# Kernel optimization log

Hardware: AMD Instinct MI355X
Metric: run time of the kernel (lower is better)

## Reference

```python
import jax, jax.numpy as jnp
import numpy as np

SIZE = 161          # odd box size (init arg 160 -> 161)
INPUT_SIZE = 8
BATCH = 256
MARGIN = 3          # VOXEL_SPREAD_MARGIN


def _radial_expansion(grid):
    # verbatim numpy port of SparseVolumeReconstructionLinear.radial_expansion
    bz = grid.shape[0]
    bz2 = bz // 2
    mask1 = grid == -1
    ls = np.linspace(-bz2, bz2, bz)
    lsx = np.linspace(0, bz2, bz // 2 + 1)
    z, y, x = np.meshgrid(ls, ls, lsx)
    c = np.zeros((int(np.sum(mask1)), 3))
    c[:, 0] = x[mask1]
    c[:, 1] = y[mask1]
    c[:, 2] = z[mask1]
    norm = np.sqrt(np.sum(np.square(c), axis=1))
    c_ = np.round(c / norm[:, None]).astype(int)
    c = c.astype(int)
    c[:, 1:] += bz2
    c_ = c - c_
    g = grid[c_[:, 2], c_[:, 1], c_[:, 0]]
    mask2 = g >= 0
    grid[c[mask2, 2], c[mask2, 1], c[mask2, 0]] = g[mask2]


def _build_grid3d_index(size):
    bz = size
    bz_2 = bz // 2
    zz = (np.arange(bz) - bz_2) ** 2
    yy = (np.arange(bz) - bz_2) ** 2
    xx = np.arange(bz_2 + 1) ** 2
    mask = (zz[:, None, None] + yy[None, :, None] + xx[None, None, :]) <= bz_2 ** 2
    # C-order enumeration matches grid_iterator(z, y, x) ordering
    idx = np.cumsum(mask.ravel()).reshape(mask.shape) - 1
    grid = np.where(mask, idx, -1).astype(np.int64)
    m = MARGIN
    bzm = bz + 2 * m
    gm = np.full((bzm, bzm, bzm // 2 + 1), -1, dtype=np.int64)
    gm[m:-m, m:-m, :-m] = grid
    for _ in range(5):
        _radial_expansion(gm)
    return gm, int(mask.sum())


def _rand_rotations(key, n):
    q = jax.random.normal(key, (n, 4))
    q = q / jnp.linalg.norm(q, axis=1, keepdims=True)
    w, x, y, z = q[:, 0], q[:, 1], q[:, 2], q[:, 3]
    R = jnp.stack([
        1 - 2 * (y * y + z * z), 2 * (x * y - z * w), 2 * (x * z + y * w),
        2 * (x * y + z * w), 1 - 2 * (x * x + z * z), 2 * (y * z - x * w),
        2 * (x * z - y * w), 2 * (y * z + x * w), 1 - 2 * (x * x + y * y),
    ], axis=-1).reshape(n, 3, 3)
    return R.astype(jnp.float32)


def setup_inputs() -> dict:
    key = jax.random.key(0)
    k1, k2, k3, k4 = jax.random.split(key, 4)
    grid3d_index, weight_count = _build_grid3d_index(SIZE)
    weight = jax.random.normal(k1, (weight_count, INPUT_SIZE, 2), dtype=jnp.float32) * 1e-3
    bias = jax.random.normal(k2, (weight_count, 2), dtype=jnp.float32) * 1e-3
    inp = jax.random.normal(k3, (BATCH, INPUT_SIZE), dtype=jnp.float32)
    rot = _rand_rotations(k4, BATCH)
    # half-plane 2D Fourier coords (x >= 0), P = SIZE * (SIZE//2 + 1)
    ys, xs = np.meshgrid(np.arange(SIZE) - SIZE // 2, np.arange(SIZE // 2 + 1), indexing='ij')
    coord = np.stack([xs.ravel(), ys.ravel()], axis=-1).astype(np.float32)
    return {
        'input': inp,
        'weight': weight,
        'bias': bias,
        'grid3d_index': jnp.asarray(grid3d_index),
        'rot_matrices': rot,
        'grid2d_coord': jnp.asarray(coord),
        'max_r': SIZE // 2,
    }


def reference(input, weight, bias, grid3d_index, rot_matrices, grid2d_coord, max_r):
    # input: (B, D); weight: (W, D, 2); bias: (W, 2)
    # grid2d_coord: (P, 2) as (x, y); rot_matrices: (B, 3, 3)
    bz = grid3d_index.shape[0]
    bz2 = bz // 2
    mr = min(int(max_r), (bz - 2 * MARGIN) // 2)
    P = grid2d_coord.shape[0]
    # rotate the z=0 plane into 3D Fourier space: (B, P, 3) as (x, y, z)
    c2 = jnp.pad(grid2d_coord, ((0, 0), (0, 1)))
    c = jnp.einsum('bij,pj->bpi', rot_matrices, c2)
    # Hermitian symmetry: flip to x >= 0 half-grid, conjugate
    flip = c[..., 0] < 0
    c = jnp.where(flip[..., None], -c, c)
    valid = jnp.sum(grid2d_coord ** 2, axis=-1) <= float(mr * mr)  # (P,)
    c = jnp.where(valid[None, :, None], c, 0.0)
    f = jnp.floor(c)
    t = c - f                      # trilinear fractions (B, P, 3)
    fi = f.astype(jnp.int32)
    out = jnp.zeros((c.shape[0], P, 2), dtype=input.dtype)
    for dx in (0, 1):
        wx = t[..., 0] if dx else 1.0 - t[..., 0]
        for dy in (0, 1):
            wy = t[..., 1] if dy else 1.0 - t[..., 1]
            for dz in (0, 1):
                wz = t[..., 2] if dz else 1.0 - t[..., 2]
                xi = fi[..., 0] + dx
                yi = fi[..., 1] + dy + bz2
                zi = fi[..., 2] + dz + bz2
                j = grid3d_index[zi, yi, xi]        # (B, P) voxel ids, -1 = empty
                jm = jnp.maximum(j, 0)
                v = jnp.einsum('bd,bpdc->bpc', input, weight[jm]) + bias[jm]
                v = jnp.where((j >= 0)[..., None], v, 0.0)
                out = out + (wx * wy * wz)[..., None] * v
    imag_sign = jnp.where(flip, -1.0, 1.0)
    out = out * jnp.stack([jnp.ones_like(imag_sign), imag_sign], axis=-1)
    return jnp.where(valid[None, :, None], out, 0.0)
```

## Files before the change

### kernel.cpp

```cpp
#include <hip/hip_runtime.h>

#define BZ    167
#define BZ2   83
#define NX    84
#define NCELL (BZ * BZ * NX)
#define SYC   NX
#define SZC   (NX * BZ)
#define NXC   81
#define NYC   161
#define NTX   21
#define NTZ   11
#define NBX   51

static __device__ __forceinline__ unsigned f2bf(float f) {
    unsigned u = __float_as_uint(f);
    return (u + 0x7FFFu + ((u >> 16) & 1u)) >> 16;
}
static __device__ __forceinline__ float bf_lo(unsigned u) {
    return __uint_as_float(u << 16);
}
static __device__ __forceinline__ float bf_hi(unsigned u) {
    return __uint_as_float(u & 0xFFFF0000u);
}

typedef _Float16 h2 __attribute__((ext_vector_type(2)));
static __device__ __forceinline__ h2 u2h(unsigned u) {
    union { unsigned u; h2 h; } x; x.u = u; return x.h;
}
static __device__ __forceinline__ unsigned f2h2(float a, float b) {
    union { h2 h; unsigned u; } x;
    x.h.x = (_Float16)a; x.h.y = (_Float16)b;
    return x.u;
}

__global__ __launch_bounds__(256) void pack_allh(
    const float4* __restrict__ wsrc, uint2* __restrict__ wdst, int nw4, int nbw,
    const int* __restrict__ grid, const float* __restrict__ bias,
    int4* __restrict__ garrD, int ncell, int nbg,
    const float* __restrict__ input, unsigned* __restrict__ inpk, int nin)
{
    const int bid = (int)blockIdx.x;
    if (bid < nbw) {
        const int i = bid * 256 + threadIdx.x;
        if (i >= nw4) return;
        const float4 v = wsrc[i];
        wdst[i] = make_uint2(f2h2(v.x, v.z), f2h2(v.y, v.w));
    } else if (bid < nbw + nbg) {
        const int i = (bid - nbw) * 256 + threadIdx.x;
        if (i >= ncell) return;
        const int j0 = grid[i];
        const int j1 = (i + SZC < ncell) ? grid[i + SZC] : -1;
        unsigned b0 = 0u, b1 = 0u;
        if (j0 >= 0)
            b0 = f2bf(bias[2 * j0]) | (f2bf(bias[2 * j0 + 1]) << 16);
        if (j1 >= 0)
            b1 = f2bf(bias[2 * j1]) | (f2bf(bias[2 * j1 + 1]) << 16);
        garrD[i] = make_int4(j0, (int)b0, j1, (int)b1);
    } else {
        const int i = (bid - nbw - nbg) * 256 + threadIdx.x;
        if (i >= nin) return;
        const int b = i >> 2, k = i & 3;
        inpk[i] = f2h2(input[b * 8 + 2 * k], input[b * 8 + 2 * k + 1]);
    }
}

__global__ __launch_bounds__(256, 4) void svr_dot(
    const unsigned* __restrict__ inpk,
    const unsigned* __restrict__ wpk,
    const int4*     __restrict__ garrD,
    const float*    __restrict__ rot,
    const float*    __restrict__ coord,
    const int*      __restrict__ max_r,
    float*          __restrict__ out,
    int P)
{
    const int b    = (int)blockIdx.x;
    const int lane = threadIdx.x & 63;
    const int wid  = threadIdx.x >> 6;
    const int ty   = (int)blockIdx.z * 4 + wid;
    if (ty * 4 >= NYC) return;

    const int q    = lane & 3;
    const int h    = q & 1;
    const int dxl  = q >> 1;
    const int sub  = lane >> 2;
    const int px   = (int)blockIdx.y * 4 + (sub & 3);
    const int py   = ty * 4 + (sub >> 2);
    if (px >= NXC || py >= NYC) return;
    const int p    = py * NXC + px;

    const float2 xy = *(const float2*)(coord + 2 * p);
    const float x = xy.x, y = xy.y;

    const int mr = min(max_r[0], (BZ - 6) / 2);
    const bool valid = (x * x + y * y) <= (float)(mr * mr);

    float2* o = (float2*)(out + ((size_t)b * P + p) * 2);
    if (!valid) {
        if (q == 0) *o = make_float2(0.f, 0.f);
        return;
    }

    const float* R = rot + b * 9;
    float cx = fmaf(R[1], y, R[0] * x);
    float cy = fmaf(R[4], y, R[3] * x);
    float cz = fmaf(R[7], y, R[6] * x);

    float sgn = 1.f;
    if (cx < 0.f) { cx = -cx; cy = -cy; cz = -cz; sgn = -1.f; }

    const float fx = floorf(cx), fy = floorf(cy), fz = floorf(cz);
    const float tx = cx - fx, ty2 = cy - fy, tz = cz - fz;
    const int ix = (int)fx;
    const int iy = (int)fy + BZ2;
    const int iz = (int)fz + BZ2;

    const int base0 = (iz * BZ + iy) * NX + ix + dxl;
    const int4 Gd0 = garrD[base0];
    const int4 Gd1 = garrD[base0 + SYC];

    const uint2 ihu = *(const uint2*)(inpk + b * 4 + h * 2);
    const h2 ihp0 = u2h(ihu.x);
    const h2 ihp1 = u2h(ihu.y);

    const float wxd = dxl ? tx : 1.f - tx;
    float wyz[4];
    wyz[0] = (1.f - ty2) * (1.f - tz);
    wyz[1] = ty2 * (1.f - tz);
    wyz[2] = (1.f - ty2) * tz;
    wyz[3] = ty2 * tz;

    int jraw[4]; unsigned bbl[4];
    jraw[0] = Gd0.x; bbl[0] = (unsigned)Gd0.y;
    jraw[1] = Gd1.x; bbl[1] = (unsigned)Gd1.y;
    jraw[2] = Gd0.z; bbl[2] = (unsigned)Gd0.w;
    jraw[3] = Gd1.z; bbl[3] = (unsigned)Gd1.w;

    int jj[4]; float wcl[4];
    #pragma unroll
    for (int i = 0; i < 4; ++i) {
        wcl[i] = (jraw[i] >= 0) ? wxd * wyz[i] : 0.f;
        jj[i]  = max(jraw[i], 0);
    }

    uint4 U[4];
    #pragma unroll
    for (int i = 0; i < 4; ++i)
        U[i] = *(const uint4*)(wpk + (size_t)jj[i] * 8 + h * 4);

    float acc0 = 0.f, acc1 = 0.f;
    #pragma unroll
    for (int i = 0; i < 4; ++i) {
        const unsigned bb = bbl[i];
        float v0 = h ? 0.f : bf_lo(bb);
        float v1 = h ? 0.f : bf_hi(bb);
        v0 = __builtin_amdgcn_fdot2(ihp0, u2h(U[i].x), v0, false);
        v0 = __builtin_amdgcn_fdot2(ihp1, u2h(U[i].z), v0, false);
        v1 = __builtin_amdgcn_fdot2(ihp0, u2h(U[i].y), v1, false);
        v1 = __builtin_amdgcn_fdot2(ihp1, u2h(U[i].w), v1, false);
        acc0 = fmaf(wcl[i], v0, acc0);
        acc1 = fmaf(wcl[i], v1, acc1);
    }

    acc0 += __shfl_xor(acc0, 1);
    acc1 += __shfl_xor(acc1, 1);
    acc0 += __shfl_xor(acc0, 2);
    acc1 += __shfl_xor(acc1, 2);

    if (q == 0) *o = make_float2(acc0, acc1 * sgn);
}

__global__ __launch_bounds__(256) void pack_w(
    const float4* __restrict__ src, uint2* __restrict__ dst, int n)
{
    const int i = blockIdx.x * 256 + threadIdx.x;
    if (i >= n) return;
    const float4 v = src[i];
    dst[i] = make_uint2(f2bf(v.x) | (f2bf(v.y) << 16),
                        f2bf(v.z) | (f2bf(v.w) << 16));
}
__global__ __launch_bounds__(256) void pack_b(
    const float* __restrict__ bias, unsigned* __restrict__ bpk, int W)
{
    const int j = blockIdx.x * 256 + threadIdx.x;
    if (j >= W) return;
    bpk[j] = f2bf(bias[2 * j]) | (f2bf(bias[2 * j + 1]) << 16);
}

__global__ __launch_bounds__(256) void svr_bf16(
    const float* __restrict__ input, const unsigned* __restrict__ wpk,
    const unsigned* __restrict__ bpk, const int* __restrict__ grid3d,
    const float* __restrict__ rot, const float* __restrict__ coord,
    const int* __restrict__ max_r, float* __restrict__ out, int P)
{
    const int m    = blockIdx.x;
    const int xcd  = m & 7;
    const int slot = m >> 3;
    const int b    = (slot / NBX) * 8 + xcd;
    const int p    = (slot % NBX) * 256 + threadIdx.x;
    if (p >= P) return;

    const float x = coord[2 * p + 0];
    const float y = coord[2 * p + 1];
    const int mr = min(max_r[0], (BZ - 6) / 2);
    const bool valid = (x * x + y * y) <= (float)(mr * mr);
    float2* o = (float2*)(out + ((size_t)b * P + p) * 2);
    if (!valid) { *o = make_float2(0.f, 0.f); return; }

    const float* R = rot + b * 9;
    float cx = fmaf(R[1], y, R[0] * x);
    float cy = fmaf(R[4], y, R[3] * x);
    float cz = fmaf(R[7], y, R[6] * x);
    float sgn = 1.f;
    if (cx < 0.f) { cx = -cx; cy = -cy; cz = -cz; sgn = -1.f; }
    const float fx = floorf(cx), fy = floorf(cy), fz = floorf(cz);
    const float tx = cx - fx, ty = cy - fy, tz = cz - fz;
    const int ix = (int)fx, iy = (int)fy + BZ2, iz = (int)fz + BZ2;

    const float* ib = input + b * 8;
    const float in0 = ib[0], in1 = ib[1], in2 = ib[2], in3 = ib[3];
    const float in4 = ib[4], in5 = ib[5], in6 = ib[6], in7 = ib[7];

    int jj[8]; float wc[8];
    const float wx0 = 1.f - tx, wy0 = 1.f - ty, wz0 = 1.f - tz;
    #pragma unroll
    for (int dz = 0; dz < 2; ++dz)
        #pragma unroll
        for (int dy = 0; dy < 2; ++dy) {
            const int base = ((iz + dz) * BZ + (iy + dy)) * NX + ix;
            #pragma unroll
            for (int dx = 0; dx < 2; ++dx) {
                const int c = dz * 4 + dy * 2 + dx;
                const int j = grid3d[base + dx];
                const float w = (dx ? tx : wx0) * (dy ? ty : wy0) * (dz ? tz : wz0);
                wc[c] = (j >= 0) ? w : 0.f;
                jj[c] = max(j, 0);
            }
        }

    uint4 U0[8], U1[8]; unsigned BB[8];
    #pragma unroll
    for (int c = 0; c < 8; ++c) {
        const uint4* wp = (const uint4*)(wpk + (size_t)jj[c] * 8);
        U0[c] = wp[0]; U1[c] = wp[1]; BB[c] = bpk[jj[c]];
    }

    float acc0 = 0.f, acc1 = 0.f;
    #pragma unroll
    for (int c = 0; c < 8; ++c) {
        const float w = wc[c];
        float v0 = bf_lo(BB[c]), v1 = bf_hi(BB[c]);
        v0 = fmaf(in0, bf_lo(U0[c].x), v0); v1 = fmaf(in0, bf_hi(U0[c].x), v1);
        v0 = fmaf(in1, bf_lo(U0[c].y), v0); v1 = fmaf(in1, bf_hi(U0[c].y), v1);
        v0 = fmaf(in2, bf_lo(U0[c].z), v0); v1 = fmaf(in2, bf_hi(U0[c].z), v1);
        v0 = fmaf(in3, bf_lo(U0[c].w), v0); v1 = fmaf(in3, bf_hi(U0[c].w), v1);
        v0 = fmaf(in4, bf_lo(U1[c].x), v0); v1 = fmaf(in4, bf_hi(U1[c].x), v1);
        v0 = fmaf(in5, bf_lo(U1[c].y), v0); v1 = fmaf(in5, bf_hi(U1[c].y), v1);
        v0 = fmaf(in6, bf_lo(U1[c].z), v0); v1 = fmaf(in6, bf_hi(U1[c].z), v1);
        v0 = fmaf(in7, bf_lo(U1[c].w), v0); v1 = fmaf(in7, bf_hi(U1[c].w), v1);
        acc0 = fmaf(w, v0, acc0);
        acc1 = fmaf(w, v1, acc1);
    }
    *o = make_float2(acc0, acc1 * sgn);
}

__global__ __launch_bounds__(256) void svr_fp32(
    const float* __restrict__ input, const float* __restrict__ weight,
    const float* __restrict__ bias, const int* __restrict__ grid3d,
    const float* __restrict__ rot, const float* __restrict__ coord,
    const int* __restrict__ max_r, float* __restrict__ out, int P)
{
    const int m    = blockIdx.x;
    const int xcd  = m & 7;
    const int slot = m >> 3;
    const int b    = (slot / NBX) * 8 + xcd;
    const int p    = (slot % NBX) * 256 + threadIdx.x;
    if (p >= P) return;

    const float x = coord[2 * p + 0];
    const float y = coord[2 * p + 1];
    const int mr = min(max_r[0], (BZ - 6) / 2);
    const bool valid = (x * x + y * y) <= (float)(mr * mr);
    float2* o = (float2*)(out + ((size_t)b * P + p) * 2);
    if (!valid) { *o = make_float2(0.f, 0.f); return; }

    const float* R = rot + b * 9;
    float cx = fmaf(R[1], y, R[0] * x);
    float cy = fmaf(R[4], y, R[3] * x);
    float cz = fmaf(R[7], y, R[6] * x);
    float sgn = 1.f;
    if (cx < 0.f) { cx = -cx; cy = -cy; cz = -cz; sgn = -1.f; }
    const float fx = floorf(cx), fy = floorf(cy), fz = floorf(cz);
    const float tx = cx - fx, ty = cy - fy, tz = cz - fz;
    const int ix = (int)fx, iy = (int)fy + BZ2, iz = (int)fz + BZ2;

    const float* ib = input + b * 8;
    const float in0 = ib[0], in1 = ib[1], in2 = ib[2], in3 = ib[3];
    const float in4 = ib[4], in5 = ib[5], in6 = ib[6], in7 = ib[7];

    int jj[8]; float wc[8];
    const float wx0 = 1.f - tx, wy0 = 1.f - ty, wz0 = 1.f - tz;
    #pragma unroll
    for (int dz = 0; dz < 2; ++dz)
        #pragma unroll
        for (int dy = 0; dy < 2; ++dy) {
            const int base = ((iz + dz) * BZ + (iy + dy)) * NX + ix;
            #pragma unroll
            for (int dx = 0; dx < 2; ++dx) {
                const int c = dz * 4 + dy * 2 + dx;
                const int j = grid3d[base + dx];
                const float w = (dx ? tx : wx0) * (dy ? ty : wy0) * (dz ? tz : wz0);
                wc[c] = (j >= 0) ? w : 0.f;
                jj[c] = max(j, 0);
            }
        }

    float acc0 = 0.f, acc1 = 0.f;
    #pragma unroll
    for (int c = 0; c < 8; ++c) {
        const size_t j = (size_t)jj[c];
        const float4* wp = (const float4*)(weight + j * 16);
        const float4 W0 = wp[0], W1 = wp[1], W2 = wp[2], W3 = wp[3];
        const float2 bb = *(const float2*)(bias + j * 2);
        const float w = wc[c];
        float v0 = bb.x, v1 = bb.y;
        v0 = fmaf(in0, W0.x, v0); v1 = fmaf(in0, W0.y, v1);
        v0 = fmaf(in1, W0.z, v0); v1 = fmaf(in1, W0.w, v1);
        v0 = fmaf(in2, W1.x, v0); v1 = fmaf(in2, W1.y, v1);
        v0 = fmaf(in3, W1.z, v0); v1 = fmaf(in3, W1.w, v1);
        v0 = fmaf(in4, W2.x, v0); v1 = fmaf(in4, W2.y, v1);
        v0 = fmaf(in5, W2.z, v0); v1 = fmaf(in5, W2.w, v1);
        v0 = fmaf(in6, W3.x, v0); v1 = fmaf(in6, W3.y, v1);
        v0 = fmaf(in7, W3.z, v0); v1 = fmaf(in7, W3.w, v1);
        acc0 = fmaf(w, v0, acc0);
        acc1 = fmaf(w, v1, acc1);
    }
    *o = make_float2(acc0, acc1 * sgn);
}

extern "C" void kernel_launch(void* const* d_in, const int* in_sizes, int n_in,
                              void* d_out, int out_size, void* d_ws, size_t ws_size,
                              hipStream_t stream) {
    const float* input  = (const float*)d_in[0];
    const float* weight = (const float*)d_in[1];
    const float* bias   = (const float*)d_in[2];
    const int*   grid3d = (const int*)  d_in[3];
    const float* rot    = (const float*)d_in[4];
    const float* coord  = (const float*)d_in[5];
    const int*   max_r  = (const int*)  d_in[6];
    float* out = (float*)d_out;

    const int P = in_sizes[5] / 2;
    const int B = in_sizes[4] / 9;
    const int W = in_sizes[1] / 16;

    const size_t wpk_bytes  = (size_t)W * 32;
    const size_t garr_bytes = (size_t)NCELL * 16;
    const size_t in_bytes   = (size_t)B * 16;
    const size_t need_zd    = wpk_bytes + garr_bytes + in_bytes;
    const size_t need_bf    = (size_t)W * 36;

    dim3 block(256, 1, 1);

    if (ws_size >= need_zd && P == NXC * NYC) {
        unsigned* wpk = (unsigned*)d_ws;
        int4* garrD = (int4*)((char*)d_ws + wpk_bytes);
        unsigned* inpk = (unsigned*)((char*)d_ws + wpk_bytes + garr_bytes);
        const int nw4 = W * 4;
        const int nbw = (nw4 + 255) / 256;
        const int nbg = (NCELL + 255) / 256;
        const int nin = B * 4;
        const int nbi = (nin + 255) / 256;
        pack_allh<<<nbw + nbg + nbi, block, 0, stream>>>(
            (const float4*)weight, (uint2*)wpk, nw4, nbw,
            grid3d, bias, garrD, NCELL, nbg,
            input, inpk, nin);
        dim3 grid(B, NTX, NTZ);
        svr_dot<<<grid, block, 0, stream>>>(inpk, wpk, garrD, rot, coord,
                                            max_r, out, P);
    } else if (ws_size >= need_bf) {
        unsigned* wpk = (unsigned*)d_ws;
        unsigned* bpk = wpk + (size_t)W * 8;
        const int nw = W * 4;
        pack_w<<<(nw + 255) / 256, block, 0, stream>>>(
            (const float4*)weight, (uint2*)wpk, nw);
        pack_b<<<(W + 255) / 256, block, 0, stream>>>(bias, bpk, W);
        dim3 grid(NBX * B, 1, 1);
        svr_bf16<<<grid, block, 0, stream>>>(input, wpk, bpk, grid3d, rot,
                                             coord, max_r, out, P);
    } else {
        dim3 grid(NBX * B, 1, 1);
        svr_fp32<<<grid, block, 0, stream>>>(input, weight, bias, grid3d, rot,
                                             coord, max_r, out, P);
    }
}
```

Measured before the change: 224.8 us.

## Shrink voxel table to int2 and remap blocks to XCDs by batch

```diff
diff --git a/kernel.cpp b/kernel.cpp
--- a/kernel.cpp
+++ b/kernel.cpp
@@ -9,7 +9,9 @@
 #define NXC   81
 #define NYC   161
 #define NTX   21
-#define NTZ   11
+#define NTY   41
+#define NTILE (NTX * NTY)
+#define NBT   216
 #define NBX   51
 
 static __device__ __forceinline__ unsigned f2bf(float f) {
@@ -33,10 +35,10 @@
     return x.u;
 }
 
-__global__ __launch_bounds__(256) void pack_allh(
+__global__ __launch_bounds__(256) void pack_td(
     const float4* __restrict__ wsrc, uint2* __restrict__ wdst, int nw4, int nbw,
     const int* __restrict__ grid, const float* __restrict__ bias,
-    int4* __restrict__ garrD, int ncell, int nbg,
+    int2* __restrict__ garr, int ncell, int nbg,
     const float* __restrict__ input, unsigned* __restrict__ inpk, int nin)
 {
     const int bid = (int)blockIdx.x;
@@ -48,14 +50,11 @@
     } else if (bid < nbw + nbg) {
         const int i = (bid - nbw) * 256 + threadIdx.x;
         if (i >= ncell) return;
-        const int j0 = grid[i];
-        const int j1 = (i + SZC < ncell) ? grid[i + SZC] : -1;
-        unsigned b0 = 0u, b1 = 0u;
-        if (j0 >= 0)
-            b0 = f2bf(bias[2 * j0]) | (f2bf(bias[2 * j0 + 1]) << 16);
-        if (j1 >= 0)
-            b1 = f2bf(bias[2 * j1]) | (f2bf(bias[2 * j1 + 1]) << 16);
-        garrD[i] = make_int4(j0, (int)b0, j1, (int)b1);
+        const int j = grid[i];
+        unsigned bb = 0u;
+        if (j >= 0)
+            bb = f2bf(bias[2 * j]) | (f2bf(bias[2 * j + 1]) << 16);
+        garr[i] = make_int2(j, (int)bb);
     } else {
         const int i = (bid - nbw - nbg) * 256 + threadIdx.x;
         if (i >= nin) return;
@@ -64,28 +63,32 @@
     }
 }
 
-__global__ __launch_bounds__(256, 4) void svr_dot(
+__global__ __launch_bounds__(256, 4) void svr_td(
     const unsigned* __restrict__ inpk,
     const unsigned* __restrict__ wpk,
-    const int4*     __restrict__ garrD,
+    const int2*     __restrict__ garr,
     const float*    __restrict__ rot,
     const float*    __restrict__ coord,
     const int*      __restrict__ max_r,
     float*          __restrict__ out,
     int P)
 {
-    const int b    = (int)blockIdx.x;
+    const int m    = blockIdx.x;
+    const int xcd  = m & 7;
+    const int slot = m >> 3;
+    const int b    = (slot / NBT) * 8 + xcd;
+    const int tgrp = slot % NBT;
+    const int wid  = threadIdx.x >> 6;
     const int lane = threadIdx.x & 63;
-    const int wid  = threadIdx.x >> 6;
-    const int ty   = (int)blockIdx.z * 4 + wid;
-    if (ty * 4 >= NYC) return;
+    const int t    = tgrp * 4 + wid;
+    if (t >= NTILE) return;
 
     const int q    = lane & 3;
     const int h    = q & 1;
     const int dxl  = q >> 1;
     const int sub  = lane >> 2;
-    const int px   = (int)blockIdx.y * 4 + (sub & 3);
-    const int py   = ty * 4 + (sub >> 2);
+    const int px   = (t % NTX) * 4 + (sub & 3);
+    const int py   = (t / NTX) * 4 + (sub >> 2);
     if (px >= NXC || py >= NYC) return;
     const int p    = py * NXC + px;
 
@@ -110,14 +113,17 @@
     if (cx < 0.f) { cx = -cx; cy = -cy; cz = -cz; sgn = -1.f; }
 
     const float fx = floorf(cx), fy = floorf(cy), fz = floorf(cz);
-    const float tx = cx - fx, ty2 = cy - fy, tz = cz - fz;
+    const float tx = cx - fx, ty = cy - fy, tz = cz - fz;
     const int ix = (int)fx;
     const int iy = (int)fy + BZ2;
     const int iz = (int)fz + BZ2;
 
     const int base0 = (iz * BZ + iy) * NX + ix + dxl;
-    const int4 Gd0 = garrD[base0];
-    const int4 Gd1 = garrD[base0 + SYC];
+    int2 Gl[4];
+    Gl[0] = garr[base0];
+    Gl[1] = garr[base0 + SYC];
+    Gl[2] = garr[base0 + SZC];
+    Gl[3] = garr[base0 + SZC + SYC];
 
     const uint2 ihu = *(const uint2*)(inpk + b * 4 + h * 2);
     const h2 ihp0 = u2h(ihu.x);
@@ -125,22 +131,17 @@
 
     const float wxd = dxl ? tx : 1.f - tx;
     float wyz[4];
-    wyz[0] = (1.f - ty2) * (1.f - tz);
-    wyz[1] = ty2 * (1.f - tz);
-    wyz[2] = (1.f - ty2) * tz;
-    wyz[3] = ty2 * tz;
-
-    int jraw[4]; unsigned bbl[4];
-    jraw[0] = Gd0.x; bbl[0] = (unsigned)Gd0.y;
-    jraw[1] = Gd1.x; bbl[1] = (unsigned)Gd1.y;
-    jraw[2] = Gd0.z; bbl[2] = (unsigned)Gd0.w;
-    jraw[3] = Gd1.z; bbl[3] = (unsigned)Gd1.w;
+    wyz[0] = (1.f - ty) * (1.f - tz);
+    wyz[1] = ty * (1.f - tz);
+    wyz[2] = (1.f - ty) * tz;
+    wyz[3] = ty * tz;
 
     int jj[4]; float wcl[4];
     #pragma unroll
     for (int i = 0; i < 4; ++i) {
-        wcl[i] = (jraw[i] >= 0) ? wxd * wyz[i] : 0.f;
-        jj[i]  = max(jraw[i], 0);
+        const int j = Gl[i].x;
+        wcl[i] = (j >= 0) ? wxd * wyz[i] : 0.f;
+        jj[i]  = max(j, 0);
     }
 
     uint4 U[4];
@@ -151,7 +152,7 @@
     float acc0 = 0.f, acc1 = 0.f;
     #pragma unroll
     for (int i = 0; i < 4; ++i) {
-        const unsigned bb = bbl[i];
+        const unsigned bb = (unsigned)Gl[i].y;
         float v0 = h ? 0.f : bf_lo(bb);
         float v1 = h ? 0.f : bf_hi(bb);
         v0 = __builtin_amdgcn_fdot2(ihp0, u2h(U[i].x), v0, false);
@@ -355,29 +356,29 @@
     const int W = in_sizes[1] / 16;
 
     const size_t wpk_bytes  = (size_t)W * 32;
-    const size_t garr_bytes = (size_t)NCELL * 16;
+    const size_t garr_bytes = (size_t)NCELL * 8;
     const size_t in_bytes   = (size_t)B * 16;
-    const size_t need_zd    = wpk_bytes + garr_bytes + in_bytes;
+    const size_t need_td    = wpk_bytes + garr_bytes + in_bytes;
     const size_t need_bf    = (size_t)W * 36;
 
     dim3 block(256, 1, 1);
 
-    if (ws_size >= need_zd && P == NXC * NYC) {
+    if (ws_size >= need_td && P == NXC * NYC) {
         unsigned* wpk = (unsigned*)d_ws;
-        int4* garrD = (int4*)((char*)d_ws + wpk_bytes);
+        int2* garr = (int2*)((char*)d_ws + wpk_bytes);
         unsigned* inpk = (unsigned*)((char*)d_ws + wpk_bytes + garr_bytes);
         const int nw4 = W * 4;
         const int nbw = (nw4 + 255) / 256;
         const int nbg = (NCELL + 255) / 256;
         const int nin = B * 4;
         const int nbi = (nin + 255) / 256;
-        pack_allh<<<nbw + nbg + nbi, block, 0, stream>>>(
+        pack_td<<<nbw + nbg + nbi, block, 0, stream>>>(
             (const float4*)weight, (uint2*)wpk, nw4, nbw,
-            grid3d, bias, garrD, NCELL, nbg,
+            grid3d, bias, garr, NCELL, nbg,
             input, inpk, nin);
-        dim3 grid(B, NTX, NTZ);
-        svr_dot<<<grid, block, 0, stream>>>(inpk, wpk, garrD, rot, coord,
-                                            max_r, out, P);
+        dim3 grid(NBT * B, 1, 1);
+        svr_td<<<grid, block, 0, stream>>>(inpk, wpk, garr, rot, coord,
+                                           max_r, out, P);
     } else if (ws_size >= need_bf) {
         unsigned* wpk = (unsigned*)d_ws;
         unsigned* bpk = wpk + (size_t)W * 8;
```

After: 213.4 us. -5.1%, faster.
